# Optimization experiments

Hardware: AMD Instinct MI355X
Metric: run time of the kernel (lower is better)

The kernel has to match this reference:

```python
import jax, jax.numpy as jnp
import numpy as np

N_NODES = 100000
N_USERS = 60000
N_MOVIES = 40000
N_EDGES = 1200000
D_IN = 64
D_EMB = 64


def setup_inputs() -> dict:
    key = jax.random.key(0)
    ks = jax.random.split(key, 6)
    x = jax.random.normal(ks[0], (N_NODES, D_IN), dtype=jnp.float32)
    edge_index = jax.random.randint(ks[1], (2, N_EDGES), 0, N_NODES, dtype=jnp.int64)
    # Glorot-ish init for the two GCNConv linear weights
    W1 = jax.random.normal(ks[2], (D_IN, D_EMB), dtype=jnp.float32) * (1.0 / np.sqrt(D_IN))
    b1 = jnp.zeros((D_EMB,), dtype=jnp.float32)
    W2 = jax.random.normal(ks[3], (D_EMB, D_EMB), dtype=jnp.float32) * (1.0 / np.sqrt(D_EMB))
    b2 = jnp.zeros((D_EMB,), dtype=jnp.float32)
    return {"x": x, "edge_index": edge_index, "W1": W1, "b1": b1, "W2": W2, "b2": b2}


def gcn_conv(x, W, b, src, dst):
    """PyG GCNConv: D^{-1/2}(A+I)D^{-1/2} X W + b with symmetric norm and self-loops."""
    h = x @ W  # [N, D_out]
    ones = jnp.ones(src.shape[0], dtype=h.dtype)
    # degree includes self-loop (+1)
    deg = jax.ops.segment_sum(ones, dst, num_segments=N_NODES) + 1.0
    dinv = jax.lax.rsqrt(deg)  # [N]
    coef = dinv[src] * dinv[dst]  # [E]
    agg = jax.ops.segment_sum(h[src] * coef[:, None], dst, num_segments=N_NODES)
    # self-loop contribution: norm = dinv[i]^2
    return agg + h * (dinv * dinv)[:, None] + b


def reference(x, edge_index, W1, b1, W2, b2):
    src, dst = edge_index[0], edge_index[1]
    h = gcn_conv(x, W1, b1, src, dst)
    h = jax.nn.relu(h)  # dropout is identity in eval mode
    h = gcn_conv(h, W2, b2, src, dst)
    user = h[:N_USERS]
    movie = h[N_USERS:N_USERS + N_MOVIES]
    return user, movie, h
```

## Files before the change

### kernel.cpp

```cpp
#include <hip/hip_runtime.h>

#define NN 100000
#define NE 1200000
#define DD 64
#define NPART 8
#define PSZ (NN / NPART)
#define EPB 4096
#define NCHUNK ((NE + EPB - 1) / EPB)
#define SCH 1024
#define SNB ((NN + SCH - 1) / SCH)

#define KCH3 96
#define CEH3 (NE / KCH3)
#define P3 4
#define BINS3 (NN / P3)
#define BINW3 (BINS3 / 4)
#define KSEG 4
#define KPS (KCH3 / KSEG)
#define NW4 (NN / 4)

static __device__ __forceinline__ unsigned short f2bf(float f) {
    unsigned int u = __float_as_uint(f);
    u += 0x7fffu + ((u >> 16) & 1u);
    return (unsigned short)(u >> 16);
}
static __device__ __forceinline__ float bf_lo(unsigned int u) {
    return __uint_as_float(u << 16);
}
static __device__ __forceinline__ float bf_hi(unsigned int u) {
    return __uint_as_float(u & 0xffff0000u);
}

__global__ __launch_bounds__(1024) void k_hist3(const int* __restrict__ dst,
                                                unsigned char* __restrict__ H,
                                                unsigned char* __restrict__ rank8) {
    __shared__ unsigned int bins[BINW3];
    int k = blockIdx.x >> 2;
    int p = blockIdx.x & 3;
    int t = threadIdx.x;
    for (int i = t; i < BINW3; i += 1024) bins[i] = 0u;
    __syncthreads();
    int lo = p * BINS3;
    int beg = k * CEH3;
    for (int e4 = beg + t * 4; e4 < beg + CEH3; e4 += 4096) {
        int4 d4 = *(const int4*)&dst[e4];
        int dd[4] = {d4.x, d4.y, d4.z, d4.w};
#pragma unroll
        for (int j = 0; j < 4; ++j) {
            unsigned int r = (unsigned int)(dd[j] - lo);
            if (r < (unsigned int)BINS3) {
                unsigned int sh = (r & 3u) << 3;
                unsigned int old = atomicAdd(&bins[r >> 2], 1u << sh);
                rank8[e4 + j] = (unsigned char)((old >> sh) & 0xffu);
            }
        }
    }
    __syncthreads();
    unsigned int* Hw = (unsigned int*)(H + (size_t)k * NN + lo);
    for (int i = t; i < BINW3; i += 1024) Hw[i] = bins[i];
}

__global__ __launch_bounds__(256) void k_cseg_sum(const unsigned int* __restrict__ H32,
                                                  unsigned int* __restrict__ aux) {
    int wd = blockIdx.x * 256 + threadIdx.x;
    int seg = blockIdx.y;
    if (wd >= NW4) return;
    unsigned int s = 0;
#pragma unroll
    for (int k = 0; k < KPS; ++k)
        s += H32[(size_t)(seg * KPS + k) * NW4 + wd];
    aux[seg * NW4 + wd] = s;
}

__global__ __launch_bounds__(256) void k_cseg_scan(unsigned int* __restrict__ H32,
                                                   const unsigned int* __restrict__ aux,
                                                   int* __restrict__ degi) {
    int wd = blockIdx.x * 256 + threadIdx.x;
    int seg = blockIdx.y;
    if (wd >= NW4) return;
    unsigned int base = 0;
    for (int i = 0; i < seg; ++i) base += aux[i * NW4 + wd];
    unsigned int s = base;
#pragma unroll
    for (int k = 0; k < KPS; ++k) {
        size_t idx = (size_t)(seg * KPS + k) * NW4 + wd;
        unsigned int v = H32[idx];
        H32[idx] = s;
        s += v;
    }
    if (seg == KSEG - 1) {
        int4 dg;
        dg.x = (int)(s & 0xffu);
        dg.y = (int)((s >> 8) & 0xffu);
        dg.z = (int)((s >> 16) & 0xffu);
        dg.w = (int)(s >> 24);
        *(int4*)&degi[4 * wd] = dg;
    }
}

__global__ __launch_bounds__(256) void k_fill3(const int* __restrict__ src,
                                               const int* __restrict__ dst,
                                               const unsigned char* __restrict__ rank8,
                                               const unsigned char* __restrict__ H,
                                               const int* __restrict__ rowptr,
                                               int* __restrict__ csr) {
    int e4 = (blockIdx.x * 256 + threadIdx.x) * 4;
    if (e4 >= NE) return;
    int4 d4 = *(const int4*)&dst[e4];
    int4 s4 = *(const int4*)&src[e4];
    unsigned int r4 = *(const unsigned int*)&rank8[e4];
    int dd[4] = {d4.x, d4.y, d4.z, d4.w};
    int ss[4] = {s4.x, s4.y, s4.z, s4.w};
    int k = e4 / CEH3;
#pragma unroll
    for (int j = 0; j < 4; ++j) {
        int d = dd[j];
        int base = rowptr[d] + (int)H[(size_t)k * NN + d];
        csr[base + (int)((r4 >> (8 * j)) & 0xffu)] = ss[j];
    }
}

__global__ void k_hist_rank(const int* __restrict__ dst, int* __restrict__ degi,
                            int* __restrict__ rank, int ne) {
    int i = blockIdx.x * blockDim.x + threadIdx.x;
    if (i < ne) rank[i] = atomicAdd(&degi[dst[i]], 1);
}

__global__ __launch_bounds__(256) void k_hist(const int* __restrict__ dst,
                                              int* __restrict__ degi, int ne) {
    int part = blockIdx.x & (NPART - 1);
    int lo = part * PSZ, hi = lo + PSZ;
    int beg = (blockIdx.x >> 3) * EPB;
    int end = min(beg + EPB, ne);
    for (int e = beg + (int)threadIdx.x; e < end; e += 256) {
        int d = dst[e];
        if (d >= lo && d < hi) atomicAdd(&degi[d], 1);
    }
}

__global__ __launch_bounds__(256) void k_scan_local(const int* __restrict__ degi,
                                                    int* __restrict__ rowptr,
                                                    int* __restrict__ part,
                                                    float* __restrict__ dinv) {
    __shared__ int wsum[4];
    int t = threadIdx.x;
    int idx = blockIdx.x * SCH + t * 4;
    int d0 = 0, d1 = 0, d2 = 0, d3 = 0;
    if (idx + 3 < NN) {
        int4 v = *(const int4*)&degi[idx];
        d0 = v.x; d1 = v.y; d2 = v.z; d3 = v.w;
        float4 dv;
        dv.x = rsqrtf((float)d0 + 1.0f);
        dv.y = rsqrtf((float)d1 + 1.0f);
        dv.z = rsqrtf((float)d2 + 1.0f);
        dv.w = rsqrtf((float)d3 + 1.0f);
        *(float4*)&dinv[idx] = dv;
    } else {
        if (idx     < NN) { d0 = degi[idx];     dinv[idx]     = rsqrtf((float)d0 + 1.0f); }
        if (idx + 1 < NN) { d1 = degi[idx + 1]; dinv[idx + 1] = rsqrtf((float)d1 + 1.0f); }
        if (idx + 2 < NN) { d2 = degi[idx + 2]; dinv[idx + 2] = rsqrtf((float)d2 + 1.0f); }
        if (idx + 3 < NN) { d3 = degi[idx + 3]; dinv[idx + 3] = rsqrtf((float)d3 + 1.0f); }
    }
    int s = d0 + d1 + d2 + d3;
    int lane = t & 63;
    int incl = s;
#pragma unroll
    for (int off = 1; off < 64; off <<= 1) {
        int v = __shfl_up(incl, off);
        if (lane >= off) incl += v;
    }
    int wv = t >> 6;
    if (lane == 63) wsum[wv] = incl;
    __syncthreads();
    int woff = 0;
#pragma unroll
    for (int i = 0; i < 4; ++i) if (i < wv) woff += wsum[i];
    int excl = woff + incl - s;
    if (idx     < NN) rowptr[idx]     = excl;
    if (idx + 1 < NN) rowptr[idx + 1] = excl + d0;
    if (idx + 2 < NN) rowptr[idx + 2] = excl + d0 + d1;
    if (idx + 3 < NN) rowptr[idx + 3] = excl + d0 + d1 + d2;
    if (t == 255) part[blockIdx.x] = woff + incl;
}

__global__ __launch_bounds__(128) void k_scan_part(int* __restrict__ part) {
    __shared__ int sm[128];
    int t = threadIdx.x;
    int v = (t < SNB) ? part[t] : 0;
    sm[t] = v;
    __syncthreads();
    for (int off = 1; off < 128; off <<= 1) {
        int add = (t >= off) ? sm[t - off] : 0;
        __syncthreads();
        sm[t] += add;
        __syncthreads();
    }
    if (t < SNB) part[t] = sm[t] - v;
}

__global__ void k_scan_add(int* __restrict__ rowptr, const int* __restrict__ part) {
    int i = blockIdx.x * blockDim.x + threadIdx.x;
    if (i < NN) rowptr[i] += part[i >> 10];
    if (i == 0) rowptr[NN] = NE;
}

__global__ void k_fill_rank(const int* __restrict__ src, const int* __restrict__ dst,
                            const int* __restrict__ rank, const int* __restrict__ rowptr,
                            int* __restrict__ csr_src, int ne) {
    int e = blockIdx.x * blockDim.x + threadIdx.x;
    if (e < ne) csr_src[rowptr[dst[e]] + rank[e]] = src[e];
}

__global__ __launch_bounds__(256) void k_fill(const int* __restrict__ src,
                                              const int* __restrict__ dst,
                                              const int* __restrict__ rowptr,
                                              int* __restrict__ cnt,
                                              int* __restrict__ csr_src, int ne) {
    int part = blockIdx.x & (NPART - 1);
    int lo = part * PSZ, hi = lo + PSZ;
    int beg = (blockIdx.x >> 3) * EPB;
    int end = min(beg + EPB, ne);
    for (int e = beg + (int)threadIdx.x; e < end; e += 256) {
        int d = dst[e];
        if (d >= lo && d < hi) {
            int pos = rowptr[d] + atomicAdd(&cnt[d], 1);
            csr_src[pos] = src[e];
        }
    }
}

__global__ __launch_bounds__(256) void k_gemm_bf(const float* __restrict__ X,
                                                 const float* __restrict__ W,
                                                 unsigned short* __restrict__ Hb,
                                                 int nrows) {
    __shared__ float4 Ws4[64][16];
    __shared__ float  Xs[64][68];
    int tid = threadIdx.x;
    const float4* W4 = (const float4*)W;
    for (int i = tid; i < 64 * 16; i += 256) Ws4[i >> 4][i & 15] = W4[i];
    int row0 = blockIdx.x * 64;
    const float4* X4 = (const float4*)X;
    for (int i = tid; i < 64 * 16; i += 256) {
        int r = i >> 4, q = i & 15;
        int row = row0 + r;
        float4 v = make_float4(0.f, 0.f, 0.f, 0.f);
        if (row < nrows) v = X4[row * 16 + q];
        *((float4*)&Xs[r][q * 4]) = v;
    }
    __syncthreads();
    int c4 = tid & 15;
    int rg = tid >> 4;
    float4 acc0 = make_float4(0.f, 0.f, 0.f, 0.f);
    float4 acc1 = acc0, acc2 = acc0, acc3 = acc0;
#pragma unroll 4
    for (int k = 0; k < 64; ++k) {
        float4 w = Ws4[k][c4];
        float x0 = Xs[rg * 4 + 0][k];
        float x1 = Xs[rg * 4 + 1][k];
        float x2 = Xs[rg * 4 + 2][k];
        float x3 = Xs[rg * 4 + 3][k];
        acc0.x += x0 * w.x; acc0.y += x0 * w.y; acc0.z += x0 * w.z; acc0.w += x0 * w.w;
        acc1.x += x1 * w.x; acc1.y += x1 * w.y; acc1.z += x1 * w.z; acc1.w += x1 * w.w;
        acc2.x += x2 * w.x; acc2.y += x2 * w.y; acc2.z += x2 * w.z; acc2.w += x2 * w.w;
        acc3.x += x3 * w.x; acc3.y += x3 * w.y; acc3.z += x3 * w.z; acc3.w += x3 * w.w;
    }
    float4 accs[4] = {acc0, acc1, acc2, acc3};
#pragma unroll
    for (int i = 0; i < 4; ++i) {
        int row = row0 + rg * 4 + i;
        if (row < nrows) {
            ushort4 o;
            o.x = f2bf(accs[i].x); o.y = f2bf(accs[i].y);
            o.z = f2bf(accs[i].z); o.w = f2bf(accs[i].w);
            *((ushort4*)&Hb[row * 64 + c4 * 4]) = o;
        }
    }
}

__global__ __launch_bounds__(256) void k_reduce(const unsigned short* __restrict__ Hb,
                                                const int* __restrict__ rowptr,
                                                const int* __restrict__ csr_src,
                                                const float* __restrict__ dinv,
                                                const float* __restrict__ b,
                                                float* __restrict__ out0,
                                                float* __restrict__ out1,
                                                int do_relu) {
    int n = blockIdx.x * 32 + (threadIdx.x >> 3);
    if (n >= NN) return;
    int cg = threadIdx.x & 7;
    float din = dinv[n];
    uint4 us = *(const uint4*)(Hb + (size_t)n * 64 + cg * 8);

    int e0 = rowptr[n];
    int deg = rowptr[n + 1] - e0;
    int dmax = deg;
    dmax = max(dmax, __shfl_xor(dmax, 8));
    dmax = max(dmax, __shfl_xor(dmax, 16));
    dmax = max(dmax, __shfl_xor(dmax, 32));

    float acc[8];
#pragma unroll
    for (int j = 0; j < 8; ++j) acc[j] = 0.f;

    bool v0 = 0 < deg;
    int s0 = v0 ? csr_src[e0] : 0;
    float cf0 = v0 ? dinv[s0] * din : 0.f;
    uint4 u0 = *(const uint4*)(Hb + (size_t)s0 * 64 + cg * 8);
    bool v1 = 1 < deg;
    int s1 = v1 ? csr_src[e0 + 1] : 0;
    float cf1 = v1 ? dinv[s1] * din : 0.f;

    for (int t = 0; t < dmax; ++t) {
        uint4 u1 = *(const uint4*)(Hb + (size_t)s1 * 64 + cg * 8);
        bool v2 = (t + 2) < deg;
        int s2 = v2 ? csr_src[e0 + t + 2] : 0;
        float cf2 = v2 ? dinv[s2] * din : 0.f;
        acc[0] += bf_lo(u0.x) * cf0;  acc[1] += bf_hi(u0.x) * cf0;
        acc[2] += bf_lo(u0.y) * cf0;  acc[3] += bf_hi(u0.y) * cf0;
        acc[4] += bf_lo(u0.z) * cf0;  acc[5] += bf_hi(u0.z) * cf0;
        acc[6] += bf_lo(u0.w) * cf0;  acc[7] += bf_hi(u0.w) * cf0;
        u0 = u1; cf0 = cf1;
        s1 = s2; cf1 = cf2;
    }

    float dd = din * din;
    float4 b0 = *(const float4*)(b + cg * 8);
    float4 b1 = *(const float4*)(b + cg * 8 + 4);
    float4 o0, o1;
    o0.x = acc[0] + bf_lo(us.x) * dd + b0.x;
    o0.y = acc[1] + bf_hi(us.x) * dd + b0.y;
    o0.z = acc[2] + bf_lo(us.y) * dd + b0.z;
    o0.w = acc[3] + bf_hi(us.y) * dd + b0.w;
    o1.x = acc[4] + bf_lo(us.z) * dd + b1.x;
    o1.y = acc[5] + bf_hi(us.z) * dd + b1.y;
    o1.z = acc[6] + bf_lo(us.w) * dd + b1.z;
    o1.w = acc[7] + bf_hi(us.w) * dd + b1.w;
    if (do_relu) {
        o0.x = fmaxf(o0.x, 0.f); o0.y = fmaxf(o0.y, 0.f);
        o0.z = fmaxf(o0.z, 0.f); o0.w = fmaxf(o0.w, 0.f);
        o1.x = fmaxf(o1.x, 0.f); o1.y = fmaxf(o1.y, 0.f);
        o1.z = fmaxf(o1.z, 0.f); o1.w = fmaxf(o1.w, 0.f);
    }
    *(float4*)(out0 + (size_t)n * 64 + cg * 8)     = o0;
    *(float4*)(out0 + (size_t)n * 64 + cg * 8 + 4) = o1;
    if (out1) {
        *(float4*)(out1 + (size_t)n * 64 + cg * 8)     = o0;
        *(float4*)(out1 + (size_t)n * 64 + cg * 8 + 4) = o1;
    }
}

__global__ void k_copy4(const float4* __restrict__ in, float4* __restrict__ out, int n4) {
    int i = blockIdx.x * blockDim.x + threadIdx.x;
    if (i < n4) out[i] = in[i];
}

extern "C" void kernel_launch(void* const* d_in, const int* in_sizes, int n_in,
                              void* d_out, int out_size, void* d_ws, size_t ws_size,
                              hipStream_t stream) {
    const float* x  = (const float*)d_in[0];
    const int*   ei = (const int*)d_in[1];
    const float* W1 = (const float*)d_in[2];
    const float* b1 = (const float*)d_in[3];
    const float* W2 = (const float*)d_in[4];
    const float* b2 = (const float*)d_in[5];
    const int* src = ei;
    const int* dst = ei + NE;

    float* A = (float*)d_out;
    float* B = (float*)d_out + (size_t)NN * DD;

    char* w = (char*)d_ws;
    size_t off = 0;
    auto alloc = [&](size_t bytes) { void* p = w + off; off += (bytes + 255) & ~(size_t)255; return p; };
    float* dinv   = (float*)alloc(NN * sizeof(float));
    int*   degi   = (int*)  alloc(NN * sizeof(int));
    int*   cnt    = (int*)  alloc(NN * sizeof(int));
    int*   rowptr = (int*)  alloc((NN + 1) * sizeof(int));
    int*   part   = (int*)  alloc(512 * sizeof(int));
    int*   csr    = (int*)  alloc(NE * sizeof(int));
    size_t off_common = off;
    void* uni = alloc((size_t)NN * DD * sizeof(unsigned short));
    size_t off_uni = off;
    size_t need_rank = off_common + (((size_t)NE * sizeof(int) + 255) & ~(size_t)255);

    bool new_path  = (ws_size >= off_uni);
    bool rank_path = !new_path && (ws_size >= need_rank);

    unsigned char* Hh    = (unsigned char*)uni;
    unsigned char* rank8 = (unsigned char*)uni + (size_t)KCH3 * NN;
    int*           rank  = (int*)uni;
    unsigned short* Bb   = new_path ? (unsigned short*)uni : (unsigned short*)B;
    bool bb_in_ws = new_path;

    if (new_path) {
        k_hist3<<<KCH3 * P3, 1024, 0, stream>>>(dst, Hh, rank8);
        dim3 cgrid((NW4 + 255) / 256, KSEG);
        k_cseg_sum<<<cgrid, 256, 0, stream>>>((unsigned int*)Hh, (unsigned int*)cnt);
        k_cseg_scan<<<cgrid, 256, 0, stream>>>((unsigned int*)Hh, (const unsigned int*)cnt, degi);
        k_scan_local<<<SNB, 256, 0, stream>>>(degi, rowptr, part, dinv);
        k_scan_part<<<1, 128, 0, stream>>>(part);
        k_scan_add<<<(NN + 255) / 256, 256, 0, stream>>>(rowptr, part);
        k_fill3<<<(NE / 4 + 255) / 256, 256, 0, stream>>>(src, dst, rank8, Hh, rowptr, csr);
    } else if (rank_path) {
        hipMemsetAsync(degi, 0, NN * sizeof(int), stream);
        k_hist_rank<<<(NE + 255) / 256, 256, 0, stream>>>(dst, degi, rank, NE);
        k_scan_local<<<SNB, 256, 0, stream>>>(degi, rowptr, part, dinv);
        k_scan_part<<<1, 128, 0, stream>>>(part);
        k_scan_add<<<(NN + 255) / 256, 256, 0, stream>>>(rowptr, part);
        k_fill_rank<<<(NE + 255) / 256, 256, 0, stream>>>(src, dst, rank, rowptr, csr, NE);
    } else {
        hipMemsetAsync(degi, 0, NN * sizeof(int), stream);
        hipMemsetAsync(cnt, 0, NN * sizeof(int), stream);
        k_hist<<<NCHUNK * NPART, 256, 0, stream>>>(dst, degi, NE);
        k_scan_local<<<SNB, 256, 0, stream>>>(degi, rowptr, part, dinv);
        k_scan_part<<<1, 128, 0, stream>>>(part);
        k_scan_add<<<(NN + 255) / 256, 256, 0, stream>>>(rowptr, part);
        k_fill<<<NCHUNK * NPART, 256, 0, stream>>>(src, dst, rowptr, cnt, csr, NE);
    }

    k_gemm_bf<<<(NN + 63) / 64, 256, 0, stream>>>(x, W1, Bb, NN);
    k_reduce<<<(NN + 31) / 32, 256, 0, stream>>>(Bb, rowptr, csr, dinv, b1, A, nullptr, 1);

    k_gemm_bf<<<(NN + 63) / 64, 256, 0, stream>>>(A, W2, Bb, NN);
    if (bb_in_ws) {
        k_reduce<<<(NN + 31) / 32, 256, 0, stream>>>(Bb, rowptr, csr, dinv, b2, A, B, 0);
    } else {
        k_reduce<<<(NN + 31) / 32, 256, 0, stream>>>(Bb, rowptr, csr, dinv, b2, A, nullptr, 0);
        k_copy4<<<(NN * DD / 4 + 255) / 256, 256, 0, stream>>>((const float4*)A, (float4*)B, NN * DD / 4);
    }
}
```

Baseline: 245.2 us.

## Precompute per-edge coefficients and deepen gather prefetch in aggregation

Adds a kernel that computes dinv[src]*dinv[dst] once per CSR edge into a coef array. Both aggregation passes then load that value instead of doing a dependent dinv gather. The aggregation loop now keeps four neighbor rows in flight instead of two, to raise memory-level parallelism. The cost is an extra launch, the coef array in the workspace, and padded iterations when the degree is not a multiple of four.

```diff
diff --git a/kernel.cpp b/kernel.cpp
--- a/kernel.cpp
+++ b/kernel.cpp
@@ -118,6 +118,17 @@
         int base = rowptr[d] + (int)H[(size_t)k * NN + d];
         csr[base + (int)((r4 >> (8 * j)) & 0xffu)] = ss[j];
     }
+}
+
+__global__ __launch_bounds__(256) void k_coef(const int* __restrict__ rowptr,
+                                              const int* __restrict__ csr,
+                                              const float* __restrict__ dinv,
+                                              float* __restrict__ coef) {
+    int n = blockIdx.x * 256 + threadIdx.x;
+    if (n >= NN) return;
+    int e = rowptr[n], end = rowptr[n + 1];
+    float dn = dinv[n];
+    for (; e < end; ++e) coef[e] = dinv[csr[e]] * dn;
 }
 
 __global__ void k_hist_rank(const int* __restrict__ dst, int* __restrict__ degi,
@@ -280,6 +291,7 @@
 __global__ __launch_bounds__(256) void k_reduce(const unsigned short* __restrict__ Hb,
                                                 const int* __restrict__ rowptr,
                                                 const int* __restrict__ csr_src,
+                                                const float* __restrict__ coef,
                                                 const float* __restrict__ dinv,
                                                 const float* __restrict__ b,
                                                 float* __restrict__ out0,
@@ -302,26 +314,32 @@
 #pragma unroll
     for (int j = 0; j < 8; ++j) acc[j] = 0.f;
 
-    bool v0 = 0 < deg;
-    int s0 = v0 ? csr_src[e0] : 0;
-    float cf0 = v0 ? dinv[s0] * din : 0.f;
-    uint4 u0 = *(const uint4*)(Hb + (size_t)s0 * 64 + cg * 8);
-    bool v1 = 1 < deg;
-    int s1 = v1 ? csr_src[e0 + 1] : 0;
-    float cf1 = v1 ? dinv[s1] * din : 0.f;
-
-    for (int t = 0; t < dmax; ++t) {
-        uint4 u1 = *(const uint4*)(Hb + (size_t)s1 * 64 + cg * 8);
-        bool v2 = (t + 2) < deg;
-        int s2 = v2 ? csr_src[e0 + t + 2] : 0;
-        float cf2 = v2 ? dinv[s2] * din : 0.f;
-        acc[0] += bf_lo(u0.x) * cf0;  acc[1] += bf_hi(u0.x) * cf0;
-        acc[2] += bf_lo(u0.y) * cf0;  acc[3] += bf_hi(u0.y) * cf0;
-        acc[4] += bf_lo(u0.z) * cf0;  acc[5] += bf_hi(u0.z) * cf0;
-        acc[6] += bf_lo(u0.w) * cf0;  acc[7] += bf_hi(u0.w) * cf0;
-        u0 = u1; cf0 = cf1;
-        s1 = s2; cf1 = cf2;
-    }
+#define LDE(T, S, C) { bool _v = (T) < deg; \
+                       S = _v ? csr_src[e0 + (T)] : 0; \
+                       C = _v ? coef[e0 + (T)] : 0.f; }
+#define GAT(U, S) U = *(const uint4*)(Hb + (size_t)(S) * 64 + cg * 8);
+#define CONS(U, C) { acc[0] += bf_lo(U.x) * (C);  acc[1] += bf_hi(U.x) * (C); \
+                     acc[2] += bf_lo(U.y) * (C);  acc[3] += bf_hi(U.y) * (C); \
+                     acc[4] += bf_lo(U.z) * (C);  acc[5] += bf_hi(U.z) * (C); \
+                     acc[6] += bf_lo(U.w) * (C);  acc[7] += bf_hi(U.w) * (C); }
+
+    int s0, s1, s2, s3; float c0, c1, c2, c3;
+    LDE(0, s0, c0); LDE(1, s1, c1); LDE(2, s2, c2); LDE(3, s3, c3);
+    uint4 u0, u1, u2, u3;
+    GAT(u0, s0); GAT(u1, s1); GAT(u2, s2); GAT(u3, s3);
+
+    for (int t = 0; t < dmax; t += 4) {
+        int sn0, sn1, sn2, sn3; float cn0, cn1, cn2, cn3;
+        LDE(t + 4, sn0, cn0); LDE(t + 5, sn1, cn1);
+        LDE(t + 6, sn2, cn2); LDE(t + 7, sn3, cn3);
+        CONS(u0, c0); GAT(u0, sn0); c0 = cn0;
+        CONS(u1, c1); GAT(u1, sn1); c1 = cn1;
+        CONS(u2, c2); GAT(u2, sn2); c2 = cn2;
+        CONS(u3, c3); GAT(u3, sn3); c3 = cn3;
+    }
+#undef LDE
+#undef GAT
+#undef CONS
 
     float dd = din * din;
     float4 b0 = *(const float4*)(b + cg * 8);
@@ -378,6 +396,7 @@
     int*   rowptr = (int*)  alloc((NN + 1) * sizeof(int));
     int*   part   = (int*)  alloc(512 * sizeof(int));
     int*   csr    = (int*)  alloc(NE * sizeof(int));
+    float* coef   = (float*)alloc(NE * sizeof(float));
     size_t off_common = off;
     void* uni = alloc((size_t)NN * DD * sizeof(unsigned short));
     size_t off_uni = off;
@@ -417,15 +436,16 @@
         k_scan_add<<<(NN + 255) / 256, 256, 0, stream>>>(rowptr, part);
         k_fill<<<NCHUNK * NPART, 256, 0, stream>>>(src, dst, rowptr, cnt, csr, NE);
     }
+    k_coef<<<(NN + 255) / 256, 256, 0, stream>>>(rowptr, csr, dinv, coef);
 
     k_gemm_bf<<<(NN + 63) / 64, 256, 0, stream>>>(x, W1, Bb, NN);
-    k_reduce<<<(NN + 31) / 32, 256, 0, stream>>>(Bb, rowptr, csr, dinv, b1, A, nullptr, 1);
+    k_reduce<<<(NN + 31) / 32, 256, 0, stream>>>(Bb, rowptr, csr, coef, dinv, b1, A, nullptr, 1);
 
     k_gemm_bf<<<(NN + 63) / 64, 256, 0, stream>>>(A, W2, Bb, NN);
     if (bb_in_ws) {
-        k_reduce<<<(NN + 31) / 32, 256, 0, stream>>>(Bb, rowptr, csr, dinv, b2, A, B, 0);
+        k_reduce<<<(NN + 31) / 32, 256, 0, stream>>>(Bb, rowptr, csr, coef, dinv, b2, A, B, 0);
     } else {
-        k_reduce<<<(NN + 31) / 32, 256, 0, stream>>>(Bb, rowptr, csr, dinv, b2, A, nullptr, 0);
+        k_reduce<<<(NN + 31) / 32, 256, 0, stream>>>(Bb, rowptr, csr, coef, dinv, b2, A, nullptr, 0);
         k_copy4<<<(NN * DD / 4 + 255) / 256, 256, 0, stream>>>((const float4*)A, (float4*)B, NN * DD / 4);
     }
 }
```

New measurement: 250.2 us. +2.0%, slower.
